# Kernel tuning notes

Measured on AMD Instinct MI355X. Metric: run time of the kernel, lower is better.

The kernel has to match this reference:

```python
import jax, jax.numpy as jnp
import numpy as np

B, N, D, H = 2, 4096, 512, 8
HD = D // H

def setup_inputs() -> dict:
    key = jax.random.key(0)
    ks = jax.random.split(key, 5)
    s = 1.0 / np.sqrt(D)
    return {
        "x": jax.random.normal(ks[0], (B, N, D), dtype=jnp.float32),
        "W_qkv": jax.random.uniform(ks[1], (D, 3 * D), minval=-s, maxval=s, dtype=jnp.float32),
        "b_qkv": jax.random.uniform(ks[2], (3 * D,), minval=-s, maxval=s, dtype=jnp.float32),
        "W_out": jax.random.uniform(ks[3], (D, D), minval=-s, maxval=s, dtype=jnp.float32),
        "b_out": jax.random.uniform(ks[4], (D,), minval=-s, maxval=s, dtype=jnp.float32),
    }

def reference(x, W_qkv, b_qkv, W_out, b_out):
    Bq, Nq, Dq = x.shape
    scale = HD ** -0.5
    qkv = x @ W_qkv + b_qkv                      # [B,N,3D]
    qkv = qkv.reshape(Bq, Nq, 3, H, HD)
    q, k, v = (jnp.moveaxis(qkv[:, :, i], 2, 1) for i in range(3))  # [B,H,N,hd]
    attn = jnp.einsum('bhqd,bhkd->bhqk', q, k) * scale   # [B,H,N,N]
    causal = jnp.tril(jnp.ones((Nq, Nq), dtype=bool))
    attn = jnp.where(causal, attn, -jnp.inf)
    attn = jax.nn.softmax(attn, axis=-1)
    out = jnp.einsum('bhqk,bhkd->bhqd', attn, v)         # [B,H,N,hd]
    out = jnp.moveaxis(out, 1, 2).reshape(Bq, Nq, Dq)
    return out @ W_out + b_out
```

## Files before the change

kernel.cpp:

```cpp
#include <hip/hip_runtime.h>
#include <hip/hip_bf16.h>


typedef __bf16 bf16_t;
typedef __bf16 bf16x4 __attribute__((ext_vector_type(4)));
typedef __bf16 bf16x8 __attribute__((ext_vector_type(8)));
typedef float  f32x4  __attribute__((ext_vector_type(4)));

__device__ __forceinline__ void gload_lds16(const bf16_t* g, bf16_t* l) {
    __builtin_amdgcn_global_load_lds(
        (const __attribute__((address_space(1))) void*)g,
        (__attribute__((address_space(3))) void*)l, 16, 0, 0);
}


__global__ void convert_f32_bf16(const float* __restrict__ in, bf16_t* __restrict__ out) {
    int i = blockIdx.x * 256 + threadIdx.x;
    float4 v = ((const float4*)in)[i];
    bf16x4 o;
    o[0] = (bf16_t)v.x; o[1] = (bf16_t)v.y; o[2] = (bf16_t)v.z; o[3] = (bf16_t)v.w;
    ((bf16x4*)out)[i] = o;
}

__global__ void transpose_tiled(const float* __restrict__ in, bf16_t* __restrict__ out, int N) {
    __shared__ bf16_t T[64][72];
    const int tid = threadIdx.x;
    const int n0 = blockIdx.x * 64, k0 = blockIdx.y * 64;
    #pragma unroll
    for (int pass = 0; pass < 4; ++pass) {
        int kk = pass * 16 + (tid >> 4), nn = (tid & 15) * 4;
        float4 v = *(const float4*)(in + (size_t)(k0 + kk) * N + n0 + nn);
        T[nn + 0][kk] = (bf16_t)v.x; T[nn + 1][kk] = (bf16_t)v.y;
        T[nn + 2][kk] = (bf16_t)v.z; T[nn + 3][kk] = (bf16_t)v.w;
    }
    __syncthreads();
    #pragma unroll
    for (int pass = 0; pass < 2; ++pass) {
        int n = pass * 32 + (tid >> 3), c8 = (tid & 7) * 8;
        *(bf16x8*)(out + (size_t)(n0 + n) * 512 + k0 + c8) = *(const bf16x8*)&T[n][c8];
    }
}

__global__ void transpose_v(const bf16_t* __restrict__ Vg, bf16_t* __restrict__ Vt) {
    __shared__ bf16_t T[64 * 64];
    const int tid = threadIdx.x;
    const int bh = blockIdx.x >> 6, n0 = (blockIdx.x & 63) * 64;
    const bf16_t* src = Vg + ((size_t)bh * 4096 + n0) * 64;
    #pragma unroll
    for (int i = 0; i < 2; ++i) {
        int c = tid + i * 256, n = c >> 3, h8 = (c & 7) * 8;
        bf16x8 v = *(const bf16x8*)(src + (size_t)n * 64 + h8);
        const int swz = (n >> 3) ^ (h8 >> 3);
        bf16_t* base = &T[swz * 8 + (n & 7)];
        #pragma unroll
        for (int j = 0; j < 8; ++j) base[(h8 + j) * 64] = v[j];
    }
    __syncthreads();
    bf16_t* dst = Vt + (size_t)bh * 64 * 4096 + n0;
    #pragma unroll
    for (int i = 0; i < 2; ++i) {
        int c = tid + i * 256, hd = c >> 3, cn = c & 7;
        *(bf16x8*)(dst + (size_t)hd * 4096 + cn * 8) =
            *(const bf16x8*)&T[hd * 64 + ((cn ^ (hd >> 3)) * 8)];
    }
}


template <int MODE, int TN>
__global__ __launch_bounds__(256) void gemm_bt(
    const bf16_t* __restrict__ A, const bf16_t* __restrict__ Bt,
    const float* __restrict__ bias,
    bf16_t* __restrict__ Qg, bf16_t* __restrict__ Kg, bf16_t* __restrict__ Vg,
    float* __restrict__ Cout)
{
    constexpr int NI = (TN == 128) ? 4 : 2;
    __shared__ bf16_t As[128 * 64];
    __shared__ bf16_t Bs[TN * 64];
    const int tid  = threadIdx.x;
    const int wid  = tid >> 6, lane = tid & 63, l16 = lane & 15, quad = lane >> 4;
    const int l8   = l16 & 7;
    const int wr   = (TN == 128) ? (wid >> 1) * 64 : wid * 32;
    const int wc   = (TN == 128) ? (wid & 1) * 64 : 0;
    const int m0   = blockIdx.y * 128, n0 = blockIdx.x * TN;

    f32x4 acc[NI][4] = {};

    for (int kk = 0; kk < 512; kk += 64) {
        __syncthreads();
        #pragma unroll
        for (int i = 0; i < 4; ++i) {
            int slot = tid + i * 256;
            int row = slot >> 3, cg = (slot & 7) ^ (row & 7);
            gload_lds16(A + (size_t)(m0 + row) * 512 + kk + cg * 8,
                        (bf16_t*)((char*)As + ((i * 256 + (wid << 6)) << 4)));
        }
        #pragma unroll
        for (int i = 0; i < TN / 32; ++i) {
            int slot = tid + i * 256;
            int row = slot >> 3, cg = (slot & 7) ^ (row & 7);
            gload_lds16(Bt + (size_t)(n0 + row) * 512 + kk + cg * 8,
                        (bf16_t*)((char*)Bs + ((i * 256 + (wid << 6)) << 4)));
        }
        __syncthreads();
        #pragma unroll
        for (int s = 0; s < 2; ++s) {
            const int sw = (s * 4 + quad);
            bf16x8 a[NI], b[4];
            #pragma unroll
            for (int i = 0; i < NI; ++i) {
                int row = wr + i * 16 + l16;
                a[i] = *(const bf16x8*)&As[(row * 8 + (sw ^ l8)) * 8];
            }
            #pragma unroll
            for (int j = 0; j < 4; ++j) {
                int row = wc + j * 16 + l16;
                b[j] = *(const bf16x8*)&Bs[(row * 8 + (sw ^ l8)) * 8];
            }
            #pragma unroll
            for (int i = 0; i < NI; ++i)
                #pragma unroll
                for (int j = 0; j < 4; ++j)
                    acc[i][j] = __builtin_amdgcn_mfma_f32_16x16x32_bf16(a[i], b[j], acc[i][j], 0, 0, 0);
        }
    }

    const float qscale = 0.18033688011112042f;
    #pragma unroll
    for (int i = 0; i < NI; ++i) {
        int mrow = m0 + wr + i * 16 + quad * 4;
        #pragma unroll
        for (int j = 0; j < 4; ++j) {
            int cgl = n0 + wc + j * 16 + l16;
            float bv = bias[cgl];
            #pragma unroll
            for (int r = 0; r < 4; ++r) {
                int m = mrow + r;
                float val = acc[i][j][r] + bv;
                if (MODE == 0) {
                    int which = cgl >> 9, hh = (cgl >> 6) & 7, hd = cgl & 63;
                    int b_ = m >> 12, n = m & 4095, bh = b_ * 8 + hh;
                    size_t idx = ((size_t)bh * 4096 + n) * 64 + hd;
                    if (which == 0)      Qg[idx] = (bf16_t)(val * qscale);
                    else if (which == 1) Kg[idx] = (bf16_t)val;
                    else                 Vg[idx] = (bf16_t)val;
                } else {
                    Cout[(size_t)m * 512 + cgl] = val;
                }
            }
        }
    }
}


__global__ __launch_bounds__(256, 3) void attn_ns2(
    const bf16_t* __restrict__ Qg, const bf16_t* __restrict__ Kg,
    const bf16_t* __restrict__ Vt,
    float* __restrict__ o_part, float* __restrict__ l_part, int nsplit)
{
    __shared__ bf16_t Ks[2][64][72];
    __shared__ bf16_t Vs[2][64][72];
    __shared__ bf16_t Ps[4][16][72];

    const int tid  = threadIdx.x;
    const int w    = tid >> 6, lane = tid & 63, l16 = lane & 15, quad = lane >> 4;
    const int bh   = blockIdx.x & 15, pr = (blockIdx.x >> 4) & 15, h = blockIdx.x >> 8;

    float* ob = o_part + (size_t)(h * 16 + bh) * 4096 * 64;
    float* lb = l_part + (size_t)(h * 16 + bh) * 4096;

    const int srow = tid >> 3, scol = (tid & 7) * 8;
    const int srow1 = srow + 32;
    const float MSHIFT = 12.0f;

    bf16x8 ones;
    #pragma unroll
    for (int j = 0; j < 8; ++j) ones[j] = (bf16_t)1.0f;

    uint4 kr0, kr1, vr0, vr1;

    for (int ph = 0; ph < 2; ++ph) {
        const int st = ph ? (31 - pr) : pr;
        const int T  = 2 * st + 2;
        const int b0 = (h * T) / nsplit, b1 = ((h + 1) * T) / nsplit;

        int qrow[2];
        bf16x8 qf[2][2];
        #pragma unroll
        for (int s = 0; s < 2; ++s) {
            qrow[s] = st * 128 + s * 64 + w * 16 + l16;
            const bf16_t* qp = Qg + ((size_t)bh * 4096 + qrow[s]) * 64;
            qf[s][0] = *(const bf16x8*)(qp + quad * 8);
            qf[s][1] = *(const bf16x8*)(qp + 32 + quad * 8);
        }

        f32x4 o[2][4] = {};
        f32x4 lacc[2] = {};

        {
            const size_t kb = ((size_t)bh * 4096 + b0 * 64) * 64;
            const size_t vb = (size_t)bh * 64 * 4096 + b0 * 64;
            kr0 = *(const uint4*)(Kg + kb + (size_t)srow * 64 + scol);
            kr1 = *(const uint4*)(Kg + kb + (size_t)srow1 * 64 + scol);
            vr0 = *(const uint4*)(Vt + vb + (size_t)srow * 4096 + scol);
            vr1 = *(const uint4*)(Vt + vb + (size_t)srow1 * 4096 + scol);
        }
        __syncthreads();

        for (int kt = b0; kt < b1; ++kt) {
            const int cur = kt & 1;
            *(uint4*)&Ks[cur][srow][scol]  = kr0;
            *(uint4*)&Ks[cur][srow1][scol] = kr1;
            *(uint4*)&Vs[cur][srow][scol]  = vr0;
            *(uint4*)&Vs[cur][srow1][scol] = vr1;
            __syncthreads();

            if (kt + 1 < b1) {
                const size_t kb = ((size_t)bh * 4096 + (kt + 1) * 64) * 64;
                const size_t vb = (size_t)bh * 64 * 4096 + (kt + 1) * 64;
                kr0 = *(const uint4*)(Kg + kb + (size_t)srow * 64 + scol);
                kr1 = *(const uint4*)(Kg + kb + (size_t)srow1 * 64 + scol);
                vr0 = *(const uint4*)(Vt + vb + (size_t)srow * 4096 + scol);
                vr1 = *(const uint4*)(Vt + vb + (size_t)srow1 * 4096 + scol);
            }

            bf16x8 kf[4][2], vf[4][2];
            #pragma unroll
            for (int cb = 0; cb < 4; ++cb) {
                kf[cb][0] = *(const bf16x8*)&Ks[cur][cb * 16 + l16][quad * 8];
                kf[cb][1] = *(const bf16x8*)&Ks[cur][cb * 16 + l16][32 + quad * 8];
            }
            #pragma unroll
            for (int j = 0; j < 4; ++j) {
                vf[j][0] = *(const bf16x8*)&Vs[cur][j * 16 + l16][quad * 8];
                vf[j][1] = *(const bf16x8*)&Vs[cur][j * 16 + l16][32 + quad * 8];
            }

            #pragma unroll
            for (int s = 0; s < 2; ++s) {
                const int diag = 2 * st + s;
                if (kt > diag) continue;

                f32x4 sv[4] = {};
                #pragma unroll
                for (int cb = 0; cb < 4; ++cb) {
                    sv[cb] = __builtin_amdgcn_mfma_f32_16x16x32_bf16(kf[cb][0], qf[s][0], sv[cb], 0, 0, 0);
                    sv[cb] = __builtin_amdgcn_mfma_f32_16x16x32_bf16(kf[cb][1], qf[s][1], sv[cb], 0, 0, 0);
                }

                if (kt == diag) {
                    #pragma unroll
                    for (int cb = 0; cb < 4; ++cb) {
                        const int keyg = kt * 64 + cb * 16 + quad * 4;
                        #pragma unroll
                        for (int r = 0; r < 4; ++r)
                            if (keyg + r > qrow[s]) sv[cb][r] = -1e30f;
                    }
                }

                #pragma unroll
                for (int cb = 0; cb < 4; ++cb) {
                    bf16x4 pk;
                    #pragma unroll
                    for (int r = 0; r < 4; ++r)
                        pk[r] = (bf16_t)__builtin_amdgcn_exp2f(sv[cb][r] - MSHIFT);
                    *(bf16x4*)&Ps[w][l16][cb * 16 + quad * 4] = pk;
                }
                bf16x8 pa0 = *(const bf16x8*)&Ps[w][l16][quad * 8];
                bf16x8 pa1 = *(const bf16x8*)&Ps[w][l16][32 + quad * 8];

                #pragma unroll
                for (int j = 0; j < 4; ++j) {
                    o[s][j] = __builtin_amdgcn_mfma_f32_16x16x32_bf16(pa0, vf[j][0], o[s][j], 0, 0, 0);
                    o[s][j] = __builtin_amdgcn_mfma_f32_16x16x32_bf16(pa1, vf[j][1], o[s][j], 0, 0, 0);
                }
                lacc[s] = __builtin_amdgcn_mfma_f32_16x16x32_bf16(pa0, ones, lacc[s], 0, 0, 0);
                lacc[s] = __builtin_amdgcn_mfma_f32_16x16x32_bf16(pa1, ones, lacc[s], 0, 0, 0);
            }
        }

        #pragma unroll
        for (int s = 0; s < 2; ++s)
            #pragma unroll
            for (int r = 0; r < 4; ++r) {
                int n = st * 128 + s * 64 + w * 16 + quad * 4 + r;
                #pragma unroll
                for (int j = 0; j < 4; ++j)
                    ob[(size_t)n * 64 + j * 16 + l16] = o[s][j][r];
                if (l16 == 0) lb[n] = lacc[s][r];
            }
    }
}

__global__ void combine_kernel(const float* __restrict__ o_part,
                               const float* __restrict__ l_part,
                               bf16_t* __restrict__ Og, int ns)
{
    int t = blockIdx.x * 256 + threadIdx.x;
    int oct = t & 7, n = (t >> 3) & 4095, bh = t >> 15;
    size_t base = ((size_t)bh * 4096 + n) * 64 + oct * 8;
    f32x4 s0 = {}, s1 = {};
    float l = 0.f;
    for (int h = 0; h < ns; ++h) {
        const float* op = o_part + (size_t)h * 16 * 4096 * 64 + base;
        s0 += *(const f32x4*)op;
        s1 += *(const f32x4*)(op + 4);
        l  += l_part[(size_t)h * 16 * 4096 + (size_t)bh * 4096 + n];
    }
    float inv = 1.0f / l;
    bf16x8 res;
    #pragma unroll
    for (int j = 0; j < 4; ++j) {
        res[j]     = (bf16_t)(s0[j] * inv);
        res[j + 4] = (bf16_t)(s1[j] * inv);
    }
    *(bf16x8*)(Og + ((size_t)((bh >> 3) * 4096 + n)) * 512 + (bh & 7) * 64 + oct * 8) = res;
}


extern "C" void kernel_launch(void* const* d_in, const int* in_sizes, int n_in,
                              void* d_out, int out_size, void* d_ws, size_t ws_size,
                              hipStream_t stream) {
    const float* x    = (const float*)d_in[0];
    const float* Wqkv = (const float*)d_in[1];
    const float* bqkv = (const float*)d_in[2];
    const float* Wout = (const float*)d_in[3];
    const float* bout = (const float*)d_in[4];
    float* out = (float*)d_out;

    char* ws = (char*)d_ws;
    bf16_t* xb  = (bf16_t*)(ws);
    bf16_t* WqT = (bf16_t*)(ws + 8388608);
    bf16_t* WoT = (bf16_t*)(ws + 9961472);
    bf16_t* Qg  = (bf16_t*)(ws + 10485760);
    bf16_t* Kg  = (bf16_t*)(ws + 18874368);
    bf16_t* Vt  = (bf16_t*)(ws + 27262976);
    bf16_t* Vg  = (bf16_t*)(ws + 35651584);

    const int nsplit = (ws_size >= 86769664ULL) ? 3 : 2;
    float* o_part = (float*)(ws + 35651584);
    float* l_part = (float*)(ws + 35651584 + (size_t)nsplit * 16777216);

    convert_f32_bf16<<<4096, 256, 0, stream>>>(x, xb);
    transpose_tiled<<<dim3(24, 8), 256, 0, stream>>>(Wqkv, WqT, 1536);
    transpose_tiled<<<dim3(8, 8), 256, 0, stream>>>(Wout, WoT, 512);

    gemm_bt<0, 128><<<dim3(12, 64), 256, 0, stream>>>(xb, WqT, bqkv, Qg, Kg, Vg, nullptr);
    transpose_v<<<1024, 256, 0, stream>>>(Vg, Vt);

    attn_ns2<<<256 * nsplit, 256, 0, stream>>>(Qg, Kg, Vt, o_part, l_part, nsplit);
    combine_kernel<<<2048, 256, 0, stream>>>(o_part, l_part, xb , nsplit);

    gemm_bt<1, 64><<<dim3(8, 64), 256, 0, stream>>>(xb, WoT, bout, nullptr, nullptr, nullptr, out);
}
```

Measured before the change: 191.0 us.

## Fuse preprocessing kernels and transpose V into LDS inside attention

Merges the x conversion and both weight transposes into one preprocess launch, and removes the separate V transpose kernel. The attention kernel now reads V in its natural [n, hd] layout and transposes it while writing into shared memory, using an XOR swizzle to limit bank conflicts. This removes two launches plus a full global read/write pass of V. In exchange, each tile does eight scalar 2-byte LDS stores per vector instead of one 16-byte store, which adds LDS work inside the attention loop.

```diff
diff --git a/kernel.cpp b/kernel.cpp
--- a/kernel.cpp
+++ b/kernel.cpp
@@ -14,18 +14,28 @@
 }
 
 
-__global__ void convert_f32_bf16(const float* __restrict__ in, bf16_t* __restrict__ out) {
-    int i = blockIdx.x * 256 + threadIdx.x;
-    float4 v = ((const float4*)in)[i];
-    bf16x4 o;
-    o[0] = (bf16_t)v.x; o[1] = (bf16_t)v.y; o[2] = (bf16_t)v.z; o[3] = (bf16_t)v.w;
-    ((bf16x4*)out)[i] = o;
-}
-
-__global__ void transpose_tiled(const float* __restrict__ in, bf16_t* __restrict__ out, int N) {
+__global__ void preprocess(const float* __restrict__ x, bf16_t* __restrict__ xb,
+                           const float* __restrict__ Wqkv, bf16_t* __restrict__ WqT,
+                           const float* __restrict__ Wout, bf16_t* __restrict__ WoT)
+{
     __shared__ bf16_t T[64][72];
     const int tid = threadIdx.x;
-    const int n0 = blockIdx.x * 64, k0 = blockIdx.y * 64;
+    const int b = blockIdx.x;
+
+    if (b < 4096) {
+        int i = b * 256 + tid;
+        float4 v = ((const float4*)x)[i];
+        bf16x4 o;
+        o[0] = (bf16_t)v.x; o[1] = (bf16_t)v.y; o[2] = (bf16_t)v.z; o[3] = (bf16_t)v.w;
+        ((bf16x4*)xb)[i] = o;
+        return;
+    }
+
+    const float* in; bf16_t* out; int N, bx, by;
+    if (b < 4288) { int t = b - 4096; in = Wqkv; out = WqT; N = 1536; bx = t % 24; by = t / 24; }
+    else          { int t = b - 4288; in = Wout; out = WoT; N = 512;  bx = t & 7;  by = t >> 3; }
+
+    const int n0 = bx * 64, k0 = by * 64;
     #pragma unroll
     for (int pass = 0; pass < 4; ++pass) {
         int kk = pass * 16 + (tid >> 4), nn = (tid & 15) * 4;
@@ -38,30 +48,6 @@
     for (int pass = 0; pass < 2; ++pass) {
         int n = pass * 32 + (tid >> 3), c8 = (tid & 7) * 8;
         *(bf16x8*)(out + (size_t)(n0 + n) * 512 + k0 + c8) = *(const bf16x8*)&T[n][c8];
-    }
-}
-
-__global__ void transpose_v(const bf16_t* __restrict__ Vg, bf16_t* __restrict__ Vt) {
-    __shared__ bf16_t T[64 * 64];
-    const int tid = threadIdx.x;
-    const int bh = blockIdx.x >> 6, n0 = (blockIdx.x & 63) * 64;
-    const bf16_t* src = Vg + ((size_t)bh * 4096 + n0) * 64;
-    #pragma unroll
-    for (int i = 0; i < 2; ++i) {
-        int c = tid + i * 256, n = c >> 3, h8 = (c & 7) * 8;
-        bf16x8 v = *(const bf16x8*)(src + (size_t)n * 64 + h8);
-        const int swz = (n >> 3) ^ (h8 >> 3);
-        bf16_t* base = &T[swz * 8 + (n & 7)];
-        #pragma unroll
-        for (int j = 0; j < 8; ++j) base[(h8 + j) * 64] = v[j];
-    }
-    __syncthreads();
-    bf16_t* dst = Vt + (size_t)bh * 64 * 4096 + n0;
-    #pragma unroll
-    for (int i = 0; i < 2; ++i) {
-        int c = tid + i * 256, hd = c >> 3, cn = c & 7;
-        *(bf16x8*)(dst + (size_t)hd * 4096 + cn * 8) =
-            *(const bf16x8*)&T[hd * 64 + ((cn ^ (hd >> 3)) * 8)];
     }
 }
 
@@ -154,7 +140,7 @@
 
 __global__ __launch_bounds__(256, 3) void attn_ns2(
     const bf16_t* __restrict__ Qg, const bf16_t* __restrict__ Kg,
-    const bf16_t* __restrict__ Vt,
+    const bf16_t* __restrict__ Vg,
     float* __restrict__ o_part, float* __restrict__ l_part, int nsplit)
 {
     __shared__ bf16_t Ks[2][64][72];
@@ -197,12 +183,11 @@
         f32x4 lacc[2] = {};
 
         {
-            const size_t kb = ((size_t)bh * 4096 + b0 * 64) * 64;
-            const size_t vb = (size_t)bh * 64 * 4096 + b0 * 64;
-            kr0 = *(const uint4*)(Kg + kb + (size_t)srow * 64 + scol);
-            kr1 = *(const uint4*)(Kg + kb + (size_t)srow1 * 64 + scol);
-            vr0 = *(const uint4*)(Vt + vb + (size_t)srow * 4096 + scol);
-            vr1 = *(const uint4*)(Vt + vb + (size_t)srow1 * 4096 + scol);
+            const size_t gb = ((size_t)bh * 4096 + b0 * 64) * 64;
+            kr0 = *(const uint4*)(Kg + gb + (size_t)srow * 64 + scol);
+            kr1 = *(const uint4*)(Kg + gb + (size_t)srow1 * 64 + scol);
+            vr0 = *(const uint4*)(Vg + gb + (size_t)srow * 64 + scol);
+            vr1 = *(const uint4*)(Vg + gb + (size_t)srow1 * 64 + scol);
         }
         __syncthreads();
 
@@ -210,17 +195,23 @@
             const int cur = kt & 1;
             *(uint4*)&Ks[cur][srow][scol]  = kr0;
             *(uint4*)&Ks[cur][srow1][scol] = kr1;
-            *(uint4*)&Vs[cur][srow][scol]  = vr0;
-            *(uint4*)&Vs[cur][srow1][scol] = vr1;
+            {
+                union { uint4 u; bf16_t hx[8]; } uv;
+                uv.u = vr0;
+                #pragma unroll
+                for (int j = 0; j < 8; ++j) Vs[cur][scol + j][srow ^ scol] = uv.hx[j];
+                uv.u = vr1;
+                #pragma unroll
+                for (int j = 0; j < 8; ++j) Vs[cur][scol + j][srow1 ^ scol] = uv.hx[j];
+            }
             __syncthreads();
 
             if (kt + 1 < b1) {
-                const size_t kb = ((size_t)bh * 4096 + (kt + 1) * 64) * 64;
-                const size_t vb = (size_t)bh * 64 * 4096 + (kt + 1) * 64;
-                kr0 = *(const uint4*)(Kg + kb + (size_t)srow * 64 + scol);
-                kr1 = *(const uint4*)(Kg + kb + (size_t)srow1 * 64 + scol);
-                vr0 = *(const uint4*)(Vt + vb + (size_t)srow * 4096 + scol);
-                vr1 = *(const uint4*)(Vt + vb + (size_t)srow1 * 4096 + scol);
+                const size_t gb = ((size_t)bh * 4096 + (kt + 1) * 64) * 64;
+                kr0 = *(const uint4*)(Kg + gb + (size_t)srow * 64 + scol);
+                kr1 = *(const uint4*)(Kg + gb + (size_t)srow1 * 64 + scol);
+                vr0 = *(const uint4*)(Vg + gb + (size_t)srow * 64 + scol);
+                vr1 = *(const uint4*)(Vg + gb + (size_t)srow1 * 64 + scol);
             }
 
             bf16x8 kf[4][2], vf[4][2];
@@ -231,8 +222,9 @@
             }
             #pragma unroll
             for (int j = 0; j < 4; ++j) {
-                vf[j][0] = *(const bf16x8*)&Vs[cur][j * 16 + l16][quad * 8];
-                vf[j][1] = *(const bf16x8*)&Vs[cur][j * 16 + l16][32 + quad * 8];
+                const int hd = j * 16 + l16, hsw = hd & 56;
+                vf[j][0] = *(const bf16x8*)&Vs[cur][hd][(quad * 8) ^ hsw];
+                vf[j][1] = *(const bf16x8*)&Vs[cur][hd][(32 + quad * 8) ^ hsw];
             }
 
             #pragma unroll
@@ -333,21 +325,17 @@
     bf16_t* WoT = (bf16_t*)(ws + 9961472);
     bf16_t* Qg  = (bf16_t*)(ws + 10485760);
     bf16_t* Kg  = (bf16_t*)(ws + 18874368);
-    bf16_t* Vt  = (bf16_t*)(ws + 27262976);
-    bf16_t* Vg  = (bf16_t*)(ws + 35651584);
+    bf16_t* Vg  = (bf16_t*)(ws + 27262976);
 
     const int nsplit = (ws_size >= 86769664ULL) ? 3 : 2;
     float* o_part = (float*)(ws + 35651584);
     float* l_part = (float*)(ws + 35651584 + (size_t)nsplit * 16777216);
 
-    convert_f32_bf16<<<4096, 256, 0, stream>>>(x, xb);
-    transpose_tiled<<<dim3(24, 8), 256, 0, stream>>>(Wqkv, WqT, 1536);
-    transpose_tiled<<<dim3(8, 8), 256, 0, stream>>>(Wout, WoT, 512);
+    preprocess<<<4352, 256, 0, stream>>>(x, xb, Wqkv, WqT, Wout, WoT);
 
     gemm_bt<0, 128><<<dim3(12, 64), 256, 0, stream>>>(xb, WqT, bqkv, Qg, Kg, Vg, nullptr);
-    transpose_v<<<1024, 256, 0, stream>>>(Vg, Vt);
-
-    attn_ns2<<<256 * nsplit, 256, 0, stream>>>(Qg, Kg, Vt, o_part, l_part, nsplit);
+
+    attn_ns2<<<256 * nsplit, 256, 0, stream>>>(Qg, Kg, Vg, o_part, l_part, nsplit);
     combine_kernel<<<2048, 256, 0, stream>>>(o_part, l_part, xb , nsplit);
 
     gemm_bt<1, 64><<<dim3(8, 64), 256, 0, stream>>>(xb, WoT, bout, nullptr, nullptr, nullptr, out);
```

Result: no change. 194.6 us (+1.9%).
